# Kernel optimization log

Hardware: AMD Instinct MI355X
Metric: run time of the kernel (lower is better)

Reference implementation:

```python
import jax, jax.numpy as jnp
import numpy as np

D = 512; H = 8; DH = D // H; NB = 4; DMLP = 2048; L = 32; ROPE_DIM = 32
SCALE = DH ** -0.25  # scale_exponent = -0.25, applied to both q and k
EPS = 1e-6


def _rms(x, g):
    return x * jax.lax.rsqrt(jnp.mean(x * x, axis=-1, keepdims=True) + EPS) * g


def _rope_tables(T):
    inv = 1.0 / (10000.0 ** (jnp.arange(0, ROPE_DIM, 2, dtype=jnp.float32) / ROPE_DIM))
    ang = jnp.arange(T, dtype=jnp.float32)[:, None] * inv[None, :]  # (T, ROPE_DIM/2)
    return jnp.cos(ang), jnp.sin(ang)


def _apply_rope(x, cos, sin):
    # x: (N, H, T, DH); rotate first ROPE_DIM dims, interleaved pairs
    xr, rest = x[..., :ROPE_DIM], x[..., ROPE_DIM:]
    x1, x2 = xr[..., 0::2], xr[..., 1::2]
    c = cos[None, None]; s = sin[None, None]
    r1 = x1 * c - x2 * s
    r2 = x1 * s + x2 * c
    rot = jnp.stack([r1, r2], axis=-1).reshape(xr.shape)
    return jnp.concatenate([rot, rest], axis=-1)


def _mha(q_in, kv_in, wq, wk, bk, wv, wo, rope=None):
    # q_in: (N, Lq, D), kv_in: (N, Lk, D); k has bias, q/v/o do not
    N, Lq, _ = q_in.shape
    Lk = kv_in.shape[1]
    q = (q_in @ wq).reshape(N, Lq, H, DH).transpose(0, 2, 1, 3)
    k = (kv_in @ wk + bk).reshape(N, Lk, H, DH).transpose(0, 2, 1, 3)
    v = (kv_in @ wv).reshape(N, Lk, H, DH).transpose(0, 2, 1, 3)
    if rope is not None:
        cos, sin = rope
        q = _apply_rope(q, cos, sin)
        k = _apply_rope(k, cos, sin)
    scores = jnp.einsum('nhqd,nhkd->nhqk', q * SCALE, k * SCALE)
    a = jax.nn.softmax(scores, axis=-1)
    o = jnp.einsum('nhqk,nhkd->nhqd', a, v).transpose(0, 2, 1, 3).reshape(N, Lq, D)
    return o @ wo


def _geglu_mlp(x, w1, w2):
    h = x @ w1                       # (..., 2*DMLP)
    a, g = jnp.split(h, 2, axis=-1)
    return (a * jax.nn.gelu(g)) @ w2


def setup_inputs() -> dict:
    key = jax.random.key(0)
    ks = jax.random.split(key, 16)
    w = lambda k, shape: jax.random.normal(k, shape, dtype=jnp.float32) * 0.02
    B, T, C = 8, 128, 64
    return {
        'source': jax.random.normal(ks[0], (B * T, C, D), dtype=jnp.float32),
        'query_latents': jax.random.normal(ks[1], (L, D), dtype=jnp.float32),
        'ca_ln': jnp.ones((NB, 3, D), jnp.float32),
        'ca_wq': w(ks[2], (NB, D, D)), 'ca_wk': w(ks[3], (NB, D, D)),
        'ca_bk': jnp.zeros((NB, D), jnp.float32),
        'ca_wv': w(ks[4], (NB, D, D)), 'ca_wo': w(ks[5], (NB, D, D)),
        'ca_w1': w(ks[6], (NB, D, 2 * DMLP)), 'ca_w2': w(ks[7], (NB, DMLP, D)),
        'ta_ln': jnp.ones((NB, 2, D), jnp.float32),
        'ta_wq': w(ks[8], (NB, D, D)), 'ta_wk': w(ks[9], (NB, D, D)),
        'ta_bk': jnp.zeros((NB, D), jnp.float32),
        'ta_wv': w(ks[10], (NB, D, D)), 'ta_wo': w(ks[11], (NB, D, D)),
        'ta_w1': w(ks[12], (NB, D, 2 * DMLP)), 'ta_w2': w(ks[13], (NB, DMLP, D)),
        'B': B, 'T': T,
    }


def reference(source, query_latents, ca_ln, ca_wq, ca_wk, ca_bk, ca_wv, ca_wo,
              ca_w1, ca_w2, ta_ln, ta_wq, ta_wk, ta_bk, ta_wv, ta_wo, ta_w1,
              ta_w2, B, T):
    BT = source.shape[0]
    rope = _rope_tables(T)
    latents = jnp.broadcast_to(query_latents[None], (BT, L, D))
    for b in range(NB):
        # --- PerceiverResamplerBlock (spatial cross-attn) ---
        l_n = _rms(latents, ca_ln[b, 0])
        s_n = _rms(source, ca_ln[b, 1])
        kv = jnp.concatenate([s_n, l_n], axis=1)  # (BT, C+L, D)
        latents = latents + _mha(l_n, kv, ca_wq[b], ca_wk[b], ca_bk[b], ca_wv[b], ca_wo[b])
        latents = latents + _geglu_mlp(_rms(latents, ca_ln[b, 2]), ca_w1[b], ca_w2[b])
        # --- TemporalAttentionBlock: (B T) L D -> (B L) T D ---
        x = latents.reshape(B, T, L, D).transpose(0, 2, 1, 3).reshape(B * L, T, D)
        x_n = _rms(x, ta_ln[b, 0])
        x = x + _mha(x_n, x_n, ta_wq[b], ta_wk[b], ta_bk[b], ta_wv[b], ta_wo[b], rope=rope)
        x = x + _geglu_mlp(_rms(x, ta_ln[b, 1]), ta_w1[b], ta_w2[b])
        latents = x.reshape(B, L, T, D).transpose(0, 2, 1, 3).reshape(BT, L, D)
    # '(B T) L D -> B T (L D)'
    return latents.reshape(B, T, L * D)
```

## Files before the change

kernel.cpp:

```cpp
#include <hip/hip_runtime.h>
#include <stdint.h>


typedef short    bf16x8 __attribute__((ext_vector_type(8)));
typedef float    f32x4  __attribute__((ext_vector_type(4)));
typedef uint16_t u16;

__device__ __forceinline__ float bf2f(uint32_t u) {
  union { uint32_t i; float f; } x; x.i = u << 16; return x.f;
}
__device__ __forceinline__ u16 f2bf(float f) {
  union { float f; uint32_t i; } x; x.f = f;
  return (u16)((x.i + 0x7fffu + ((x.i >> 16) & 1u)) >> 16);
}
__device__ __forceinline__ float gelu_t(float x) {
  float u = 0.7978845608028654f * (x + 0.044715f * x * x * x);
  float t = 1.f - 2.f / (__expf(2.f * u) + 1.f);
  return 0.5f * x * (1.f + t);
}
template<int RMAP>
__device__ __forceinline__ int maprow(int r) {
  if (RMAP == 0) return r;
  int b = r >> 12, rem = r & 4095;
  return ((b << 7) + (rem & 127)) * 32 + (rem >> 7);
}
__device__ __forceinline__ void glds16(const u16* g, u16* l) {
  __builtin_amdgcn_global_load_lds((const __attribute__((address_space(1))) uint32_t*)(g),
                                   (__attribute__((address_space(3))) uint32_t*)(l),
                                   16, 0, 0);
}

__global__ __launch_bounds__(256) void transpose_cast(const float* __restrict__ src,
                                                      u16* __restrict__ dst,
                                                      int R, int C, size_t zsD) {
  src += (size_t)blockIdx.z * R * C;
  dst += (size_t)blockIdx.z * zsD;
  __shared__ float t[32][33];
  int c0 = blockIdx.x * 32, r0 = blockIdx.y * 32;
  int tx = threadIdx.x & 31, ty = threadIdx.x >> 5;
#pragma unroll
  for (int i = 0; i < 32; i += 8) t[ty + i][tx] = src[(size_t)(r0 + ty + i) * C + c0 + tx];
  __syncthreads();
#pragma unroll
  for (int i = 0; i < 32; i += 8)
    dst[(size_t)(c0 + ty + i) * R + r0 + tx] = f2bf(t[tx][ty + i]);
}

__global__ __launch_bounds__(256) void transpose_w1(const float* __restrict__ src,
                                                    u16* __restrict__ dst) {
  src += (size_t)blockIdx.z * 512 * 4096;
  dst += (size_t)blockIdx.z * 512 * 4096;
  __shared__ float t[32][33];
  int c0 = blockIdx.x * 32, r0 = blockIdx.y * 32;
  int m0 = (c0 >> 8) * 128 + ((c0 >> 6) & 3) * 32 + ((c0 & 32) ? 2048 : 0);
  int tx = threadIdx.x & 31, ty = threadIdx.x >> 5;
#pragma unroll
  for (int i = 0; i < 32; i += 8) t[ty + i][tx] = src[(size_t)(r0 + ty + i) * 4096 + m0 + tx];
  __syncthreads();
#pragma unroll
  for (int i = 0; i < 32; i += 8)
    dst[(size_t)(c0 + ty + i) * 512 + r0 + tx] = f2bf(t[tx][ty + i]);
}

__global__ void rope_init(float* cosT, float* sinT) {
  int idx = blockIdx.x * 256 + threadIdx.x;
  if (idx < 128 * 16) {
    int t = idx >> 4, j = idx & 15;
    float inv = __expf(-logf(10000.f) * (float)j / 16.f);
    float a = (float)t * inv;
    cosT[idx] = cosf(a);
    sinT[idx] = sinf(a);
  }
}

__global__ __launch_bounds__(256) void init_lat(const float* __restrict__ ql,
                                                float* __restrict__ lat) {
  size_t i = (size_t)blockIdx.x * 256 + threadIdx.x;
  int r = (int)(i >> 7), cw = (int)(i & 127);
  int l = r & 31;
  ((float4*)lat)[i] = ((const float4*)ql)[l * 128 + cw];
}

template<int RMAP>
__global__ __launch_bounds__(256) void rms_rows(const float* __restrict__ src,
                                                const float* __restrict__ g,
                                                u16* __restrict__ out) {
  const int wid = threadIdx.x >> 6, lane = threadIdx.x & 63;
  const int row = (blockIdx.x << 2) + wid;
  const int srow = maprow<RMAP>(row);
  const float4* p = (const float4*)(src + (size_t)srow * 512);
  float4 v0 = p[lane * 2], v1 = p[lane * 2 + 1];
  float ss = v0.x * v0.x + v0.y * v0.y + v0.z * v0.z + v0.w * v0.w +
             v1.x * v1.x + v1.y * v1.y + v1.z * v1.z + v1.w * v1.w;
#pragma unroll
  for (int m = 1; m < 64; m <<= 1) ss += __shfl_xor(ss, m);
  const float rs = rsqrtf(ss * (1.f / 512.f) + 1e-6f);
  const float4* gp = (const float4*)g;
  float4 g0 = gp[lane * 2], g1 = gp[lane * 2 + 1];
  u16 rb[8];
  rb[0] = f2bf(v0.x * rs * g0.x); rb[1] = f2bf(v0.y * rs * g0.y);
  rb[2] = f2bf(v0.z * rs * g0.z); rb[3] = f2bf(v0.w * rs * g0.w);
  rb[4] = f2bf(v1.x * rs * g1.x); rb[5] = f2bf(v1.y * rs * g1.y);
  rb[6] = f2bf(v1.z * rs * g1.z); rb[7] = f2bf(v1.w * rs * g1.w);
  *(int4*)(out + (size_t)row * 512 + lane * 8) = *(int4*)rb;
}

template<int EPI, int RMAP, int AMAP>
__global__ __launch_bounds__(512, 2) void gemm256(const u16* __restrict__ A,
                                                  const u16* __restrict__ A2,
                                                  const u16* __restrict__ Bt,
                                                  u16* __restrict__ outH,
                                                  float* __restrict__ latF,
                                                  const float* __restrict__ bias,
                                                  int M, int N, int K, int nb) {
  __shared__ __align__(16) u16 Ab[3][256 * 64];
  __shared__ __align__(16) u16 Bb[2][256 * 64];
  const int tid = threadIdx.x;
  const int nwg = gridDim.x * gridDim.y;
  int bid = blockIdx.y * gridDim.x + blockIdx.x;
  bid = (bid & 7) * (nwg >> 3) + (bid >> 3);
  const int m0 = (bid / gridDim.x) << 8;
  const int n0 = (bid % gridDim.x) << 8;
  const int wid = tid >> 6, lane = tid & 63;
  const int wm = wid >> 2, wn = wid & 3;
  const int lr = lane & 15, lg = lane >> 4;
  const int rx = (lr & 7) << 3;

  auto stageA = [&](int slot, int kt, int h) {
#pragma unroll
    for (int i = 0; i < 2; ++i) {
      const int e = ((h * 2 + i) * 512 + tid) * 8;
      const int r = e >> 6;
      const int cs = (e & 63) ^ ((r & 7) << 3);
      const u16* src;
      if constexpr (AMAP == 0) {
        src = A + (size_t)(m0 + r) * K + kt * 64 + cs;
      } else {
        const int R = m0 + r;
        const int n_ = R / 96;
        const int j = R - n_ * 96;
        src = (j < 64) ? A  + ((size_t)((nb + n_) * 64 + j)) * 512 + kt * 64 + cs
                       : A2 + ((size_t)((nb + n_) * 32 + (j - 64))) * 512 + kt * 64 + cs;
      }
      glds16(src, &Ab[slot][e]);
    }
  };
  auto stageB = [&](int slot, int kt, int h) {
#pragma unroll
    for (int i = 0; i < 2; ++i) {
      const int e = ((h * 2 + i) * 512 + tid) * 8;
      const int r = e >> 6;
      const int cs = (e & 63) ^ ((r & 7) << 3);
      glds16(Bt + (size_t)(n0 + r) * K + kt * 64 + cs, &Bb[slot][e]);
    }
  };

  bf16x8 bfr[2][4];
  bf16x8 afrA[2][2], afrB_[2][2];
  auto readAfr = [&](bf16x8 (&dst)[2][2], const u16* Abase, int p) {
#pragma unroll
    for (int d = 0; d < 2; ++d)
#pragma unroll
      for (int ks = 0; ks < 2; ++ks) {
        const int rw = wm * 128 + (p * 2 + d) * 16 + lr;
        dst[d][ks] = *(const bf16x8*)&Abase[rw * 64 + ((ks * 32 + lg * 8) ^ rx)];
      }
  };
  auto readBfr = [&](const u16* Bbase) {
#pragma unroll
    for (int ks = 0; ks < 2; ++ks)
#pragma unroll
      for (int in = 0; in < 4; ++in) {
        const int rw = wn * 64 + in * 16 + lr;
        bfr[ks][in] = *(const bf16x8*)&Bbase[rw * 64 + ((ks * 32 + lg * 8) ^ rx)];
      }
  };

  f32x4 acc[8][4];
#pragma unroll
  for (int i = 0; i < 8; ++i)
#pragma unroll
    for (int j = 0; j < 4; ++j) acc[i][j] = (f32x4){0.f, 0.f, 0.f, 0.f};

  stageA(0, 0, 0); stageA(0, 0, 1);
  stageB(0, 0, 0); stageB(0, 0, 1);
  stageA(1, 1, 0); stageA(1, 1, 1);
  asm volatile("s_waitcnt vmcnt(4)" ::: "memory");
  __builtin_amdgcn_s_barrier();
  asm volatile("" ::: "memory");
  readBfr(&Bb[0][0]);
  readAfr(afrA, &Ab[0][0], 0);

  const int nkt = K >> 6;
  int sl0 = 0;
  int sl2 = 2;
  for (int kt = 0; kt < nkt; ++kt) {
    const u16* Abase = &Ab[sl0][0];
#pragma unroll
    for (int p = 0; p < 4; ++p) {
      if (p <= 1 && kt + 1 < nkt) stageB((kt + 1) & 1, kt + 1, p);
      if (p >= 2 && kt + 2 < nkt) stageA(sl2, kt + 2, p - 2);
      if (p < 3) {
        if ((p & 1) == 0) readAfr(afrB_, Abase, p + 1);
        else              readAfr(afrA,  Abase, p + 1);
      }
      __builtin_amdgcn_s_setprio(1);
      if ((p & 1) == 0) {
#pragma unroll
        for (int d = 0; d < 2; ++d)
#pragma unroll
          for (int in = 0; in < 4; ++in)
#pragma unroll
            for (int ks = 0; ks < 2; ++ks)
              acc[p * 2 + d][in] = __builtin_amdgcn_mfma_f32_16x16x32_bf16(
                  afrA[d][ks], bfr[ks][in], acc[p * 2 + d][in], 0, 0, 0);
      } else {
#pragma unroll
        for (int d = 0; d < 2; ++d)
#pragma unroll
          for (int in = 0; in < 4; ++in)
#pragma unroll
            for (int ks = 0; ks < 2; ++ks)
              acc[p * 2 + d][in] = __builtin_amdgcn_mfma_f32_16x16x32_bf16(
                  afrB_[d][ks], bfr[ks][in], acc[p * 2 + d][in], 0, 0, 0);
      }
      __builtin_amdgcn_s_setprio(0);
      if (p < 3) {
        __builtin_amdgcn_s_barrier();
      } else if (kt + 1 < nkt) {
        if (kt + 2 < nkt) asm volatile("s_waitcnt vmcnt(4)" ::: "memory");
        else              asm volatile("s_waitcnt vmcnt(0)" ::: "memory");
        __builtin_amdgcn_s_barrier();
        asm volatile("" ::: "memory");
        const int sln = (sl0 == 2) ? 0 : sl0 + 1;
        readBfr(&Bb[(kt + 1) & 1][0]);
        readAfr(afrA, &Ab[sln][0], 0);
      }
    }
    sl0 = (sl0 == 2) ? 0 : sl0 + 1;
    sl2 = (sl2 == 2) ? 0 : sl2 + 1;
  }

  if constexpr (EPI == 3) {
    const int t128 = n0 >> 1;
#pragma unroll
    for (int im = 0; im < 8; ++im)
#pragma unroll
      for (int in = 0; in < 2; ++in)
#pragma unroll
        for (int j = 0; j < 4; ++j) {
          const int row = m0 + wm * 128 + im * 16 + lg * 4 + j;
          const int hcol = t128 + wn * 32 + in * 16 + lr;
          outH[(size_t)row * 2048 + hcol] = f2bf(acc[im][in][j] * gelu_t(acc[im][in + 2][j]));
        }
  } else if constexpr (EPI == 2) {
#pragma unroll
    for (int im = 0; im < 8; ++im)
#pragma unroll
      for (int in = 0; in < 4; ++in) {
        const int col = n0 + wn * 64 + in * 16 + lr;
#pragma unroll
        for (int j = 0; j < 4; ++j) {
          const int row = m0 + wm * 128 + im * 16 + lg * 4 + j;
          const size_t rr = (size_t)maprow<RMAP>(row) * 512 + col;
          latF[rr] += acc[im][in][j];
        }
      }
  } else {
    float bv4[4];
    if constexpr (EPI == 1) {
#pragma unroll
      for (int in = 0; in < 4; ++in)
        bv4[in] = (n0 < 512) ? bias[n0 + wn * 64 + in * 16 + lr] : 0.f;
    }
#pragma unroll
    for (int im = 0; im < 8; ++im)
#pragma unroll
      for (int in = 0; in < 4; ++in) {
        const int col = n0 + wn * 64 + in * 16 + lr;
#pragma unroll
        for (int j = 0; j < 4; ++j) {
          const int row = m0 + wm * 128 + im * 16 + lg * 4 + j;
          float v = acc[im][in][j];
          if constexpr (EPI == 1) v += bv4[in];
          outH[(size_t)row * N + col] = f2bf(v);
        }
      }
  }
}

__global__ __launch_bounds__(256) void attn_ca(const u16* q,
                                               const u16* __restrict__ kv,
                                               u16* o, int nb) {
  union __align__(16) SM {
    struct { u16 Qs[32][72]; u16 Ks[96][72]; } qk;
    u16 Pb[32][104];
  };
  __shared__ SM sm;
  __shared__ __align__(16) u16 Vt[64][104];
  __shared__ float pmax[2][32];
  __shared__ float psum[2][32];
  const int nl = blockIdx.x, n = nb + nl, h = blockIdx.y, tid = threadIdx.x;

  {
    int r = tid >> 3, c = (tid & 7) * 8;
    *(int4*)&sm.qk.Qs[r][c] = *(const int4*)&q[((size_t)n * 32 + r) * 512 + h * 64 + c];
  }
#pragma unroll
  for (int i = 0; i < 3; ++i) {
    int idx = i * 256 + tid;
    int r = idx >> 3, c = (idx & 7) * 8;
    *(int4*)&sm.qk.Ks[r][c] = *(const int4*)&kv[((size_t)nl * 96 + r) * 1024 + h * 64 + c];
  }
#pragma unroll
  for (int i = 0; i < 3; ++i) {
    int idx = i * 256 + tid;
    int dg = idx / 96, t = idx - dg * 96;
    int4 pv = *(const int4*)&kv[((size_t)nl * 96 + t) * 1024 + 512 + h * 64 + dg * 8];
    const u16* pu = (const u16*)&pv;
#pragma unroll
    for (int e = 0; e < 8; ++e) Vt[dg * 8 + e][t] = pu[e];
  }
  __syncthreads();

  const int wid = tid >> 6, lane = tid & 63, lr = lane & 15, lg = lane >> 4;
  const int m0 = (wid & 1) * 16, wnq = wid >> 1, nbc = wnq * 48;

  f32x4 sa[3];
#pragma unroll
  for (int f = 0; f < 3; ++f) sa[f] = (f32x4){0.f, 0.f, 0.f, 0.f};
#pragma unroll
  for (int ks = 0; ks < 2; ++ks) {
    bf16x8 a = *(const bf16x8*)&sm.qk.Qs[m0 + lr][ks * 32 + lg * 8];
#pragma unroll
    for (int f = 0; f < 3; ++f) {
      bf16x8 bb = *(const bf16x8*)&sm.qk.Ks[nbc + f * 16 + lr][ks * 32 + lg * 8];
      sa[f] = __builtin_amdgcn_mfma_f32_16x16x32_bf16(a, bb, sa[f], 0, 0, 0);
    }
  }

#pragma unroll
  for (int j = 0; j < 4; ++j) {
    float m = fmaxf(fmaxf(sa[0][j], sa[1][j]), sa[2][j]);
    m = fmaxf(m, __shfl_xor(m, 1));
    m = fmaxf(m, __shfl_xor(m, 2));
    m = fmaxf(m, __shfl_xor(m, 4));
    m = fmaxf(m, __shfl_xor(m, 8));
    if (lr == 0) pmax[wnq][m0 + lg * 4 + j] = m;
  }
  __syncthreads();
#pragma unroll
  for (int j = 0; j < 4; ++j) {
    const int row = m0 + lg * 4 + j;
    const float m = fmaxf(pmax[0][row], pmax[1][row]);
    float s = 0.f;
#pragma unroll
    for (int f = 0; f < 3; ++f) {
      float p = __expf(0.125f * (sa[f][j] - m));
      sa[f][j] = p;
      s += p;
    }
    s += __shfl_xor(s, 1); s += __shfl_xor(s, 2); s += __shfl_xor(s, 4); s += __shfl_xor(s, 8);
    if (lr == 0) psum[wnq][row] = s;
  }
#pragma unroll
  for (int f = 0; f < 3; ++f)
#pragma unroll
    for (int j = 0; j < 4; ++j)
      sm.Pb[m0 + lg * 4 + j][nbc + f * 16 + lr] = f2bf(sa[f][j]);
  __syncthreads();

// ... 121 lines not shown
#pragma unroll
    for (int in = 0; in < 4; ++in)
#pragma unroll
      for (int j = 0; j < 4; ++j)
        sm.Pb[rbase + im * 16 + lg * 4 + j][wn * 64 + in * 16 + lr] = f2bf(sa[im][in][j]);
  __syncthreads();

  f32x4 oa[2][4];
#pragma unroll
  for (int i = 0; i < 2; ++i)
#pragma unroll
    for (int j = 0; j < 4; ++j) oa[i][j] = (f32x4){0.f, 0.f, 0.f, 0.f};
#pragma unroll
  for (int ks = 0; ks < 4; ++ks) {
    bf16x8 av[2], bv[4];
#pragma unroll
    for (int im = 0; im < 2; ++im)
      av[im] = *(const bf16x8*)&sm.Pb[wid * 32 + im * 16 + lr][ks * 32 + lg * 8];
#pragma unroll
    for (int in = 0; in < 4; ++in)
      bv[in] = *(const bf16x8*)&Vt[in * 16 + lr][ks * 32 + lg * 8];
#pragma unroll
    for (int im = 0; im < 2; ++im)
#pragma unroll
      for (int in = 0; in < 4; ++in)
        oa[im][in] = __builtin_amdgcn_mfma_f32_16x16x32_bf16(av[im], bv[in], oa[im][in], 0, 0, 0);
  }
#pragma unroll
  for (int im = 0; im < 2; ++im)
#pragma unroll
    for (int j = 0; j < 4; ++j) {
      const int qi = wid * 32 + im * 16 + lg * 4 + j;
      const float inv = 1.f / (psum[0][qi] + psum[1][qi]);
#pragma unroll
      for (int in = 0; in < 4; ++in)
        o[((size_t)n * 128 + qi) * 512 + h * 64 + in * 16 + lr] = f2bf(oa[im][in][j] * inv);
    }
}

extern "C" void kernel_launch(void* const* d_in, const int* in_sizes, int n_in,
                              void* d_out, int out_size, void* d_ws, size_t ws_size,
                              hipStream_t stream) {
  const float* source = (const float*)d_in[0];
  const float* qlat   = (const float*)d_in[1];
  const float* ca_ln  = (const float*)d_in[2];
  const float* ca_wq  = (const float*)d_in[3];
  const float* ca_wk  = (const float*)d_in[4];
  const float* ca_bk  = (const float*)d_in[5];
  const float* ca_wv  = (const float*)d_in[6];
  const float* ca_wo  = (const float*)d_in[7];
  const float* ca_w1  = (const float*)d_in[8];
  const float* ca_w2  = (const float*)d_in[9];
  const float* ta_ln  = (const float*)d_in[10];
  const float* ta_wq  = (const float*)d_in[11];
  const float* ta_wk  = (const float*)d_in[12];
  const float* ta_bk  = (const float*)d_in[13];
  const float* ta_wv  = (const float*)d_in[14];
  const float* ta_wo  = (const float*)d_in[15];
  const float* ta_w1  = (const float*)d_in[16];
  const float* ta_w2  = (const float*)d_in[17];
  float* lat = (float*)d_out;
  char* ws = (char*)d_ws;
  (void)in_sizes; (void)n_in; (void)out_size;

  if (ws_size < 251674624ull) return;

  const size_t WQ = 512 * 512, W1SZ = (size_t)512 * 4096, W2SZ = (size_t)2048 * 512;
  const size_t O_CA_WQ = 0,
               O_CA_KV = 4 * WQ,
               O_CA_WO = 12 * WQ,
               O_CA_W1 = 16 * WQ,
               O_CA_W2 = O_CA_W1 + 4 * W1SZ,
               O_TA_WQ = O_CA_W2 + 4 * W2SZ,
               O_TA_KV = O_TA_WQ + 4 * WQ,
               O_TA_WO = O_TA_KV + 8 * WQ,
               O_TA_W1 = O_TA_WO + 4 * WQ,
               O_TA_W2 = O_TA_W1 + 4 * W1SZ;

  u16*   W    = (u16*)ws;
  u16*   xn   = (u16*)(ws + 67108864);
  u16*   shat = (u16*)(ws + 100663296);
  u16*   qb   = (u16*)(ws + 167772160);
  u16*   kvb  = (u16*)(ws + 201326592);
  u16*   h2   = shat;
  u16*   takv = shat;
  float* cosT = (float*)(ws + 251658240);
  float* sinT = (float*)(ws + 251666432);

  transpose_cast<<<dim3(16, 16, 4), 256, 0, stream>>>(ca_wq, W + O_CA_WQ, 512, 512, WQ);
  transpose_cast<<<dim3(16, 16, 4), 256, 0, stream>>>(ca_wk, W + O_CA_KV, 512, 512, 2 * WQ);
  transpose_cast<<<dim3(16, 16, 4), 256, 0, stream>>>(ca_wv, W + O_CA_KV + WQ, 512, 512, 2 * WQ);
  transpose_cast<<<dim3(16, 16, 4), 256, 0, stream>>>(ca_wo, W + O_CA_WO, 512, 512, WQ);
  transpose_w1 <<<dim3(128, 16, 4), 256, 0, stream>>>(ca_w1, W + O_CA_W1);
  transpose_cast<<<dim3(16, 64, 4), 256, 0, stream>>>(ca_w2, W + O_CA_W2, 2048, 512, W2SZ);
  transpose_cast<<<dim3(16, 16, 4), 256, 0, stream>>>(ta_wq, W + O_TA_WQ, 512, 512, WQ);
  transpose_cast<<<dim3(16, 16, 4), 256, 0, stream>>>(ta_wk, W + O_TA_KV, 512, 512, 2 * WQ);
  transpose_cast<<<dim3(16, 16, 4), 256, 0, stream>>>(ta_wv, W + O_TA_KV + WQ, 512, 512, 2 * WQ);
  transpose_cast<<<dim3(16, 16, 4), 256, 0, stream>>>(ta_wo, W + O_TA_WO, 512, 512, WQ);
  transpose_w1 <<<dim3(128, 16, 4), 256, 0, stream>>>(ta_w1, W + O_TA_W1);
  transpose_cast<<<dim3(16, 64, 4), 256, 0, stream>>>(ta_w2, W + O_TA_W2, 2048, 512, W2SZ);
  rope_init<<<8, 256, 0, stream>>>(cosT, sinT);
  init_lat<<<16384, 256, 0, stream>>>(qlat, lat);

  for (int b = 0; b < 4; ++b) {
    const u16* wqt   = W + O_CA_WQ + (size_t)b * WQ;
    const u16* wkvt  = W + O_CA_KV + (size_t)b * 2 * WQ;
    const u16* wot   = W + O_CA_WO + (size_t)b * WQ;
    const u16* w1t   = W + O_CA_W1 + (size_t)b * W1SZ;
    const u16* w2t   = W + O_CA_W2 + (size_t)b * W2SZ;
    const u16* twqt  = W + O_TA_WQ + (size_t)b * WQ;
    const u16* twkvt = W + O_TA_KV + (size_t)b * 2 * WQ;
    const u16* twot  = W + O_TA_WO + (size_t)b * WQ;
    const u16* tw1t  = W + O_TA_W1 + (size_t)b * W1SZ;
    const u16* tw2t  = W + O_TA_W2 + (size_t)b * W2SZ;

    rms_rows<0><<<8192, 256, 0, stream>>>(lat, ca_ln + b * 1536, xn);
    rms_rows<0><<<16384, 256, 0, stream>>>(source, ca_ln + b * 1536 + 512, shat);
    gemm256<0, 0, 0><<<dim3(2, 128), 512, 0, stream>>>(xn, nullptr, wqt, qb, nullptr, nullptr, 32768, 512, 512, 0);
    for (int c = 0; c < 4; ++c) {
      gemm256<1, 0, 1><<<dim3(4, 96), 512, 0, stream>>>(shat, xn, wkvt, kvb, nullptr, ca_bk + b * 512, 24576, 1024, 512, c * 256);
      attn_ca<<<dim3(256, 8), 256, 0, stream>>>(qb, kvb, qb, c * 256);
    }
    gemm256<2, 0, 0><<<dim3(2, 128), 512, 0, stream>>>(qb, nullptr, wot, nullptr, lat, nullptr, 32768, 512, 512, 0);
    rms_rows<0><<<8192, 256, 0, stream>>>(lat, ca_ln + b * 1536 + 1024, xn);
    gemm256<3, 0, 0><<<dim3(16, 128), 512, 0, stream>>>(xn, nullptr, w1t, h2, nullptr, nullptr, 32768, 4096, 512, 0);
    gemm256<2, 0, 0><<<dim3(2, 128), 512, 0, stream>>>(h2, nullptr, w2t, nullptr, lat, nullptr, 32768, 512, 2048, 0);

    rms_rows<1><<<8192, 256, 0, stream>>>(lat, ta_ln + b * 1024, xn);
    gemm256<0, 0, 0><<<dim3(2, 128), 512, 0, stream>>>(xn, nullptr, twqt, qb, nullptr, nullptr, 32768, 512, 512, 0);
    gemm256<1, 0, 0><<<dim3(4, 128), 512, 0, stream>>>(xn, nullptr, twkvt, takv, nullptr, ta_bk + b * 512, 32768, 1024, 512, 0);
    attn_ta<<<dim3(256, 8), 256, 0, stream>>>(qb, takv, cosT, sinT, qb);
    gemm256<2, 1, 0><<<dim3(2, 128), 512, 0, stream>>>(qb, nullptr, twot, nullptr, lat, nullptr, 32768, 512, 512, 0);
    rms_rows<1><<<8192, 256, 0, stream>>>(lat, ta_ln + b * 1024 + 512, xn);
    gemm256<3, 0, 0><<<dim3(16, 128), 512, 0, stream>>>(xn, nullptr, tw1t, h2, nullptr, nullptr, 32768, 4096, 512, 0);
    gemm256<2, 1, 0><<<dim3(2, 128), 512, 0, stream>>>(h2, nullptr, tw2t, nullptr, lat, nullptr, 32768, 512, 2048, 0);
  }
}
```

Measured before the change: 4.910 ms.

## Fuse GeGLU MLP up-projection, gating and down-projection into one kernel

Replaces the two-GEMM MLP (W1 with GeGLU epilogue writing a bf16 hidden buffer, then W2 accumulating into latents) with a single kernel. Each block owns 128 rows, loops over 16 hidden chunks of 128, keeps the gated chunk in LDS and accumulates the W2 product in registers. This removes the 32768x2048 hidden tensor round-trip through global memory and one launch. In exchange the new kernel uses a simpler double-buffered pipeline with full vmcnt(0) barriers, launches only 256 blocks, and rereads the full W1/W2 weights per block.

```diff
diff --git a/kernel.cpp b/kernel.cpp
--- a/kernel.cpp
+++ b/kernel.cpp
@@ -28,6 +28,11 @@
   __builtin_amdgcn_global_load_lds((const __attribute__((address_space(1))) uint32_t*)(g),
                                    (__attribute__((address_space(3))) uint32_t*)(l),
                                    16, 0, 0);
+}
+__device__ __forceinline__ void vm0_bar() {
+  asm volatile("s_waitcnt vmcnt(0)" ::: "memory");
+  __builtin_amdgcn_s_barrier();
+  asm volatile("" ::: "memory");
 }
 
 __global__ __launch_bounds__(256) void transpose_cast(const float* __restrict__ src,
@@ -52,7 +57,7 @@
   dst += (size_t)blockIdx.z * 512 * 4096;
   __shared__ float t[32][33];
   int c0 = blockIdx.x * 32, r0 = blockIdx.y * 32;
-  int m0 = (c0 >> 8) * 128 + ((c0 >> 6) & 3) * 32 + ((c0 & 32) ? 2048 : 0);
+  int m0 = (c0 >> 8) * 128 + (((c0 >> 6) & 3)) * 32 + ((c0 >> 5) & 1) * 2048;
   int tx = threadIdx.x & 31, ty = threadIdx.x >> 5;
 #pragma unroll
   for (int i = 0; i < 32; i += 8) t[ty + i][tx] = src[(size_t)(r0 + ty + i) * 4096 + m0 + tx];
@@ -103,6 +108,141 @@
   rb[4] = f2bf(v1.x * rs * g1.x); rb[5] = f2bf(v1.y * rs * g1.y);
   rb[6] = f2bf(v1.z * rs * g1.z); rb[7] = f2bf(v1.w * rs * g1.w);
   *(int4*)(out + (size_t)row * 512 + lane * 8) = *(int4*)rb;
+}
+
+template<int RMAP>
+__global__ __launch_bounds__(512, 2) void mlp_fused(const u16* __restrict__ A,
+                                                    const u16* __restrict__ W1t,
+                                                    const u16* __restrict__ W2t,
+                                                    float* __restrict__ latF) {
+  __shared__ union __align__(16) {
+    struct { u16 Ab[2][128 * 64]; u16 B1b[2][256 * 64]; } g1;
+    struct { u16 B2b[2][512 * 32]; } g2;
+  } stg;
+  __shared__ __align__(16) u16 hb[128][136];
+  const int tid = threadIdx.x;
+  const int bid = blockIdx.x;
+  const int rb = (((bid & 7) << 5) + (bid >> 3)) << 7;
+  const int wid = tid >> 6, lane = tid & 63;
+  const int wm = wid >> 2, wn = wid & 3;
+  const int lr = lane & 15, lg = lane >> 4;
+  const int rx = (lr & 7) << 3;
+
+  auto stageA1 = [&](int bf, int kt) {
+#pragma unroll
+    for (int i = 0; i < 2; ++i) {
+      const int e = (i * 512 + tid) * 8;
+      const int r = e >> 6;
+      const int cs = (e & 63) ^ ((r & 7) << 3);
+      glds16(A + (size_t)(rb + r) * 512 + kt * 64 + cs, &stg.g1.Ab[bf][e]);
+    }
+  };
+  f32x4 acc2[4][8];
+#pragma unroll
+  for (int i = 0; i < 4; ++i)
+#pragma unroll
+    for (int j = 0; j < 8; ++j) acc2[i][j] = (f32x4){0.f, 0.f, 0.f, 0.f};
+
+  for (int c = 0; c < 16; ++c) {
+    auto stageB1 = [&](int bf, int kt) {
+#pragma unroll
+      for (int i = 0; i < 4; ++i) {
+        const int e = (i * 512 + tid) * 8;
+        const int r = e >> 6;
+        const int cs = (e & 63) ^ ((r & 7) << 3);
+        glds16(W1t + (size_t)(c * 256 + r) * 512 + kt * 64 + cs, &stg.g1.B1b[bf][e]);
+      }
+    };
+    auto stageB2 = [&](int bf, int kt2) {
+#pragma unroll
+      for (int i = 0; i < 4; ++i) {
+        const int e = (i * 512 + tid) * 8;
+        const int r = e >> 5;
+        const int cs = (e & 31) ^ (((r >> 1) & 3) << 3);
+        glds16(W2t + (size_t)r * 2048 + c * 128 + kt2 * 32 + cs, &stg.g2.B2b[bf][e]);
+      }
+    };
+
+    f32x4 acc1[4][4];
+#pragma unroll
+    for (int i = 0; i < 4; ++i)
+#pragma unroll
+      for (int j = 0; j < 4; ++j) acc1[i][j] = (f32x4){0.f, 0.f, 0.f, 0.f};
+    stageA1(0, 0); stageB1(0, 0);
+    vm0_bar();
+    for (int kt = 0; kt < 8; ++kt) {
+      const int bf = kt & 1;
+      if (kt + 1 < 8) { stageA1(bf ^ 1, kt + 1); stageB1(bf ^ 1, kt + 1); }
+      const u16* Ab_ = &stg.g1.Ab[bf][0];
+      const u16* Bb_ = &stg.g1.B1b[bf][0];
+#pragma unroll
+      for (int ks = 0; ks < 2; ++ks) {
+        bf16x8 av[4], bv[4];
+#pragma unroll
+        for (int im = 0; im < 4; ++im)
+          av[im] = *(const bf16x8*)&Ab_[(wm * 64 + im * 16 + lr) * 64 + ((ks * 32 + lg * 8) ^ rx)];
+#pragma unroll
+        for (int in = 0; in < 4; ++in)
+          bv[in] = *(const bf16x8*)&Bb_[(wn * 64 + in * 16 + lr) * 64 + ((ks * 32 + lg * 8) ^ rx)];
+        __builtin_amdgcn_s_setprio(1);
+#pragma unroll
+        for (int im = 0; im < 4; ++im)
+#pragma unroll
+          for (int in = 0; in < 4; ++in)
+            acc1[im][in] = __builtin_amdgcn_mfma_f32_16x16x32_bf16(av[im], bv[in], acc1[im][in], 0, 0, 0);
+        __builtin_amdgcn_s_setprio(0);
+      }
+      vm0_bar();
+    }
+
+#pragma unroll
+    for (int im = 0; im < 4; ++im)
+#pragma unroll
+      for (int in = 0; in < 2; ++in)
+#pragma unroll
+        for (int j = 0; j < 4; ++j) {
+          const int row = wm * 64 + im * 16 + lg * 4 + j;
+          const int hl = wn * 32 + in * 16 + lr;
+          hb[row][hl] = f2bf(acc1[im][in][j] * gelu_t(acc1[im][in + 2][j]));
+        }
+    stageB2(0, 0);
+    __syncthreads();
+
+    for (int kt2 = 0; kt2 < 4; ++kt2) {
+      const int bf = kt2 & 1;
+      if (kt2 + 1 < 4) stageB2(bf ^ 1, kt2 + 1);
+      const u16* B2_ = &stg.g2.B2b[bf][0];
+      bf16x8 av[4], bv[8];
+#pragma unroll
+      for (int im = 0; im < 4; ++im)
+        av[im] = *(const bf16x8*)&hb[wm * 64 + im * 16 + lr][kt2 * 32 + lg * 8];
+#pragma unroll
+      for (int in = 0; in < 8; ++in) {
+        const int ng = wn * 128 + in * 16 + lr;
+        bv[in] = *(const bf16x8*)&B2_[ng * 32 + ((lg * 8) ^ (((ng >> 1) & 3) << 3))];
+      }
+      __builtin_amdgcn_s_setprio(1);
+#pragma unroll
+      for (int im = 0; im < 4; ++im)
+#pragma unroll
+        for (int in = 0; in < 8; ++in)
+          acc2[im][in] = __builtin_amdgcn_mfma_f32_16x16x32_bf16(av[im], bv[in], acc2[im][in], 0, 0, 0);
+      __builtin_amdgcn_s_setprio(0);
+      vm0_bar();
+    }
+  }
+
+#pragma unroll
+  for (int im = 0; im < 4; ++im)
+#pragma unroll
+    for (int in = 0; in < 8; ++in) {
+      const int col = wn * 128 + in * 16 + lr;
+#pragma unroll
+      for (int j = 0; j < 4; ++j) {
+        const int row = rb + wm * 64 + im * 16 + lg * 4 + j;
+        latF[(size_t)maprow<RMAP>(row) * 512 + col] += acc2[im][in][j];
+      }
+    }
 }
 
 template<int EPI, int RMAP, int AMAP>
@@ -192,8 +332,7 @@
   readAfr(afrA, &Ab[0][0], 0);
 
   const int nkt = K >> 6;
-  int sl0 = 0;
-  int sl2 = 2;
+  int sl0 = 0, sl2 = 2;
   for (int kt = 0; kt < nkt; ++kt) {
     const u16* Abase = &Ab[sl0][0];
 #pragma unroll
@@ -241,19 +380,7 @@
     sl2 = (sl2 == 2) ? 0 : sl2 + 1;
   }
 
-  if constexpr (EPI == 3) {
-    const int t128 = n0 >> 1;
-#pragma unroll
-    for (int im = 0; im < 8; ++im)
-#pragma unroll
-      for (int in = 0; in < 2; ++in)
-#pragma unroll
-        for (int j = 0; j < 4; ++j) {
-          const int row = m0 + wm * 128 + im * 16 + lg * 4 + j;
-          const int hcol = t128 + wn * 32 + in * 16 + lr;
-          outH[(size_t)row * 2048 + hcol] = f2bf(acc[im][in][j] * gelu_t(acc[im][in + 2][j]));
-        }
-  } else if constexpr (EPI == 2) {
+  if constexpr (EPI == 2) {
 #pragma unroll
     for (int im = 0; im < 8; ++im)
 #pragma unroll
@@ -574,7 +701,6 @@
   u16*   shat = (u16*)(ws + 100663296);
   u16*   qb   = (u16*)(ws + 167772160);
   u16*   kvb  = (u16*)(ws + 201326592);
-  u16*   h2   = shat;
   u16*   takv = shat;
   float* cosT = (float*)(ws + 251658240);
   float* sinT = (float*)(ws + 251666432);
@@ -615,8 +741,7 @@
     }
     gemm256<2, 0, 0><<<dim3(2, 128), 512, 0, stream>>>(qb, nullptr, wot, nullptr, lat, nullptr, 32768, 512, 512, 0);
     rms_rows<0><<<8192, 256, 0, stream>>>(lat, ca_ln + b * 1536 + 1024, xn);
-    gemm256<3, 0, 0><<<dim3(16, 128), 512, 0, stream>>>(xn, nullptr, w1t, h2, nullptr, nullptr, 32768, 4096, 512, 0);
-    gemm256<2, 0, 0><<<dim3(2, 128), 512, 0, stream>>>(h2, nullptr, w2t, nullptr, lat, nullptr, 32768, 512, 2048, 0);
+    mlp_fused<0><<<256, 512, 0, stream>>>(xn, w1t, w2t, lat);
 
     rms_rows<1><<<8192, 256, 0, stream>>>(lat, ta_ln + b * 1024, xn);
     gemm256<0, 0, 0><<<dim3(2, 128), 512, 0, stream>>>(xn, nullptr, twqt, qb, nullptr, nullptr, 32768, 512, 512, 0);
@@ -624,7 +749,6 @@
     attn_ta<<<dim3(256, 8), 256, 0, stream>>>(qb, takv, cosT, sinT, qb);
     gemm256<2, 1, 0><<<dim3(2, 128), 512, 0, stream>>>(qb, nullptr, twot, nullptr, lat, nullptr, 32768, 512, 512, 0);
     rms_rows<1><<<8192, 256, 0, stream>>>(lat, ta_ln + b * 1024 + 512, xn);
-    gemm256<3, 0, 0><<<dim3(16, 128), 512, 0, stream>>>(xn, nullptr, tw1t, h2, nullptr, nullptr, 32768, 4096, 512, 0);
-    gemm256<2, 1, 0><<<dim3(2, 128), 512, 0, stream>>>(h2, nullptr, tw2t, nullptr, lat, nullptr, 32768, 512, 2048, 0);
-  }
-}
+    mlp_fused<1><<<256, 512, 0, stream>>>(xn, tw1t, tw2t, lat);
+  }
+}
```

New measurement: 6.023 ms. 1.23x slower.

## Make GEMM kernel persistent over multiple tiles with cross-tile prefetch pipeline

Applied to the files above, without the earlier changes.

Turns the 256x256 GEMM into a semi-persistent kernel where each workgroup processes TPB consecutive output tiles as one flattened virtual K loop. The next tile's A/B loads are prefetched while the current tile finishes, and the epilogue runs mid-loop before the accumulators are reset. This removes per-tile prologue and pipeline drain, and shrinks the grid to 256 or 192 workgroups, intended to match the CU count. The cost is that the epilogue stores now sit inside the pipelined loop and can stall MFMA issue. Tile order within a workgroup also changes L2 reuse.

```diff
diff --git a/kernel.cpp b/kernel.cpp
--- a/kernel.cpp
+++ b/kernel.cpp
@@ -105,28 +105,33 @@
   *(int4*)(out + (size_t)row * 512 + lane * 8) = *(int4*)rb;
 }
 
-template<int EPI, int RMAP, int AMAP>
-__global__ __launch_bounds__(512, 2) void gemm256(const u16* __restrict__ A,
-                                                  const u16* __restrict__ A2,
-                                                  const u16* __restrict__ Bt,
-                                                  u16* __restrict__ outH,
-                                                  float* __restrict__ latF,
-                                                  const float* __restrict__ bias,
-                                                  int M, int N, int K, int nb) {
+template<int EPI, int RMAP, int AMAP, int TPB>
+__global__ __launch_bounds__(512, 2) void gemm256p(const u16* __restrict__ A,
+                                                   const u16* __restrict__ A2,
+                                                   const u16* __restrict__ Bt,
+                                                   u16* __restrict__ outH,
+                                                   float* __restrict__ latF,
+                                                   const float* __restrict__ bias,
+                                                   int N, int K, int ltn, int nb) {
   __shared__ __align__(16) u16 Ab[3][256 * 64];
   __shared__ __align__(16) u16 Bb[2][256 * 64];
   const int tid = threadIdx.x;
-  const int nwg = gridDim.x * gridDim.y;
-  int bid = blockIdx.y * gridDim.x + blockIdx.x;
-  bid = (bid & 7) * (nwg >> 3) + (bid >> 3);
-  const int m0 = (bid / gridDim.x) << 8;
-  const int n0 = (bid % gridDim.x) << 8;
+  const int NBk = gridDim.x;
+  const int sb = (blockIdx.x & 7) * (NBk >> 3) + (blockIdx.x >> 3);
   const int wid = tid >> 6, lane = tid & 63;
   const int wm = wid >> 2, wn = wid & 3;
   const int lr = lane & 15, lg = lane >> 4;
   const int rx = (lr & 7) << 3;
-
-  auto stageA = [&](int slot, int kt, int h) {
+  const int nkt = K >> 6;
+  const int lnkt = __builtin_ctz(nkt);
+  const int tmask = nkt - 1;
+  const int NV = TPB * nkt;
+  const int tnm = (1 << ltn) - 1;
+
+  auto stageA = [&](int vk, int slot, int h) {
+    const int g = sb * TPB + (vk >> lnkt);
+    const int m0 = (g >> ltn) << 8;
+    const int kt = vk & tmask;
 #pragma unroll
     for (int i = 0; i < 2; ++i) {
       const int e = ((h * 2 + i) * 512 + tid) * 8;
@@ -145,7 +150,10 @@
       glds16(src, &Ab[slot][e]);
     }
   };
-  auto stageB = [&](int slot, int kt, int h) {
+  auto stageB = [&](int vk, int slot, int h) {
+    const int g = sb * TPB + (vk >> lnkt);
+    const int n0 = (g & tnm) << 8;
+    const int kt = vk & tmask;
 #pragma unroll
     for (int i = 0; i < 2; ++i) {
       const int e = ((h * 2 + i) * 512 + tid) * 8;
@@ -181,6 +189,58 @@
   for (int i = 0; i < 8; ++i)
 #pragma unroll
     for (int j = 0; j < 4; ++j) acc[i][j] = (f32x4){0.f, 0.f, 0.f, 0.f};
+
+  auto epilogue = [&](int tv) {
+    const int g = sb * TPB + tv;
+    const int m0 = (g >> ltn) << 8;
+    const int n0 = (g & tnm) << 8;
+    if constexpr (EPI == 3) {
+      const int t128 = n0 >> 1;
+#pragma unroll
+      for (int im = 0; im < 8; ++im)
+#pragma unroll
+        for (int in = 0; in < 2; ++in)
+#pragma unroll
+          for (int j = 0; j < 4; ++j) {
+            const int row = m0 + wm * 128 + im * 16 + lg * 4 + j;
+            const int hcol = t128 + wn * 32 + in * 16 + lr;
+            outH[(size_t)row * 2048 + hcol] = f2bf(acc[im][in][j] * gelu_t(acc[im][in + 2][j]));
+          }
+    } else if constexpr (EPI == 2) {
+#pragma unroll
+      for (int im = 0; im < 8; ++im)
+#pragma unroll
+        for (int in = 0; in < 4; ++in) {
+          const int col = n0 + wn * 64 + in * 16 + lr;
+#pragma unroll
+          for (int j = 0; j < 4; ++j) {
+            const int row = m0 + wm * 128 + im * 16 + lg * 4 + j;
+            const size_t rr = (size_t)maprow<RMAP>(row) * 512 + col;
+            latF[rr] += acc[im][in][j];
+          }
+        }
+    } else {
+      float bv4[4];
+      if constexpr (EPI == 1) {
+#pragma unroll
+        for (int in = 0; in < 4; ++in)
+          bv4[in] = (n0 < 512) ? bias[n0 + wn * 64 + in * 16 + lr] : 0.f;
+      }
+#pragma unroll
+      for (int im = 0; im < 8; ++im)
+#pragma unroll
+        for (int in = 0; in < 4; ++in) {
+          const int col = n0 + wn * 64 + in * 16 + lr;
+#pragma unroll
+          for (int j = 0; j < 4; ++j) {
+            const int row = m0 + wm * 128 + im * 16 + lg * 4 + j;
+            float v = acc[im][in][j];
+            if constexpr (EPI == 1) v += bv4[in];
+            outH[(size_t)row * N + col] = f2bf(v);
+          }
+        }
+    }
+  };
 
   stageA(0, 0, 0); stageA(0, 0, 1);
   stageB(0, 0, 0); stageB(0, 0, 1);
@@ -191,15 +251,13 @@
   readBfr(&Bb[0][0]);
   readAfr(afrA, &Ab[0][0], 0);
 
-  const int nkt = K >> 6;
-  int sl0 = 0;
-  int sl2 = 2;
-  for (int kt = 0; kt < nkt; ++kt) {
+  int sl0 = 0, sl2 = 2;
+  for (int vk = 0; vk < NV; ++vk) {
     const u16* Abase = &Ab[sl0][0];
 #pragma unroll
     for (int p = 0; p < 4; ++p) {
-      if (p <= 1 && kt + 1 < nkt) stageB((kt + 1) & 1, kt + 1, p);
-      if (p >= 2 && kt + 2 < nkt) stageA(sl2, kt + 2, p - 2);
+      if (p <= 1 && vk + 1 < NV) stageB(vk + 1, (vk + 1) & 1, p);
+      if (p >= 2 && vk + 2 < NV) stageA(vk + 2, sl2, p - 2);
       if (p < 3) {
         if ((p & 1) == 0) readAfr(afrB_, Abase, p + 1);
         else              readAfr(afrA,  Abase, p + 1);
@@ -227,66 +285,27 @@
       __builtin_amdgcn_s_setprio(0);
       if (p < 3) {
         __builtin_amdgcn_s_barrier();
-      } else if (kt + 1 < nkt) {
-        if (kt + 2 < nkt) asm volatile("s_waitcnt vmcnt(4)" ::: "memory");
-        else              asm volatile("s_waitcnt vmcnt(0)" ::: "memory");
+      } else if (vk + 1 < NV) {
+        if (vk + 2 < NV) asm volatile("s_waitcnt vmcnt(4)" ::: "memory");
+        else             asm volatile("s_waitcnt vmcnt(0)" ::: "memory");
         __builtin_amdgcn_s_barrier();
         asm volatile("" ::: "memory");
+        if (TPB > 1 && (vk & tmask) == tmask) {
+          epilogue(vk >> lnkt);
+#pragma unroll
+          for (int i = 0; i < 8; ++i)
+#pragma unroll
+            for (int j = 0; j < 4; ++j) acc[i][j] = (f32x4){0.f, 0.f, 0.f, 0.f};
+        }
         const int sln = (sl0 == 2) ? 0 : sl0 + 1;
-        readBfr(&Bb[(kt + 1) & 1][0]);
+        readBfr(&Bb[(vk + 1) & 1][0]);
         readAfr(afrA, &Ab[sln][0], 0);
       }
     }
     sl0 = (sl0 == 2) ? 0 : sl0 + 1;
     sl2 = (sl2 == 2) ? 0 : sl2 + 1;
   }
-
-  if constexpr (EPI == 3) {
-    const int t128 = n0 >> 1;
-#pragma unroll
-    for (int im = 0; im < 8; ++im)
-#pragma unroll
-      for (int in = 0; in < 2; ++in)
-#pragma unroll
-        for (int j = 0; j < 4; ++j) {
-          const int row = m0 + wm * 128 + im * 16 + lg * 4 + j;
-          const int hcol = t128 + wn * 32 + in * 16 + lr;
-          outH[(size_t)row * 2048 + hcol] = f2bf(acc[im][in][j] * gelu_t(acc[im][in + 2][j]));
-        }
-  } else if constexpr (EPI == 2) {
-#pragma unroll
-    for (int im = 0; im < 8; ++im)
-#pragma unroll
-      for (int in = 0; in < 4; ++in) {
-        const int col = n0 + wn * 64 + in * 16 + lr;
-#pragma unroll
-        for (int j = 0; j < 4; ++j) {
-          const int row = m0 + wm * 128 + im * 16 + lg * 4 + j;
-          const size_t rr = (size_t)maprow<RMAP>(row) * 512 + col;
-          latF[rr] += acc[im][in][j];
-        }
-      }
-  } else {
-    float bv4[4];
-    if constexpr (EPI == 1) {
-#pragma unroll
-      for (int in = 0; in < 4; ++in)
-        bv4[in] = (n0 < 512) ? bias[n0 + wn * 64 + in * 16 + lr] : 0.f;
-    }
-#pragma unroll
-    for (int im = 0; im < 8; ++im)
-#pragma unroll
-      for (int in = 0; in < 4; ++in) {
-        const int col = n0 + wn * 64 + in * 16 + lr;
-#pragma unroll
-        for (int j = 0; j < 4; ++j) {
-          const int row = m0 + wm * 128 + im * 16 + lg * 4 + j;
-          float v = acc[im][in][j];
-          if constexpr (EPI == 1) v += bv4[in];
-          outH[(size_t)row * N + col] = f2bf(v);
-        }
-      }
-  }
+  epilogue(TPB - 1);
 }
 
 __global__ __launch_bounds__(256) void attn_ca(const u16* q,
@@ -608,23 +627,23 @@
 
     rms_rows<0><<<8192, 256, 0, stream>>>(lat, ca_ln + b * 1536, xn);
     rms_rows<0><<<16384, 256, 0, stream>>>(source, ca_ln + b * 1536 + 512, shat);
-    gemm256<0, 0, 0><<<dim3(2, 128), 512, 0, stream>>>(xn, nullptr, wqt, qb, nullptr, nullptr, 32768, 512, 512, 0);
+    gemm256p<0, 0, 0, 1><<<256, 512, 0, stream>>>(xn, nullptr, wqt, qb, nullptr, nullptr, 512, 512, 1, 0);
     for (int c = 0; c < 4; ++c) {
-      gemm256<1, 0, 1><<<dim3(4, 96), 512, 0, stream>>>(shat, xn, wkvt, kvb, nullptr, ca_bk + b * 512, 24576, 1024, 512, c * 256);
+      gemm256p<1, 0, 1, 2><<<192, 512, 0, stream>>>(shat, xn, wkvt, kvb, nullptr, ca_bk + b * 512, 1024, 512, 2, c * 256);
       attn_ca<<<dim3(256, 8), 256, 0, stream>>>(qb, kvb, qb, c * 256);
     }
-    gemm256<2, 0, 0><<<dim3(2, 128), 512, 0, stream>>>(qb, nullptr, wot, nullptr, lat, nullptr, 32768, 512, 512, 0);
+    gemm256p<2, 0, 0, 1><<<256, 512, 0, stream>>>(qb, nullptr, wot, nullptr, lat, nullptr, 512, 512, 1, 0);
     rms_rows<0><<<8192, 256, 0, stream>>>(lat, ca_ln + b * 1536 + 1024, xn);
-    gemm256<3, 0, 0><<<dim3(16, 128), 512, 0, stream>>>(xn, nullptr, w1t, h2, nullptr, nullptr, 32768, 4096, 512, 0);
-    gemm256<2, 0, 0><<<dim3(2, 128), 512, 0, stream>>>(h2, nullptr, w2t, nullptr, lat, nullptr, 32768, 512, 2048, 0);
+    gemm256p<3, 0, 0, 8><<<256, 512, 0, stream>>>(xn, nullptr, w1t, h2, nullptr, nullptr, 4096, 512, 4, 0);
+    gemm256p<2, 0, 0, 1><<<256, 512, 0, stream>>>(h2, nullptr, w2t, nullptr, lat, nullptr, 512, 2048, 1, 0);
 
     rms_rows<1><<<8192, 256, 0, stream>>>(lat, ta_ln + b * 1024, xn);
-    gemm256<0, 0, 0><<<dim3(2, 128), 512, 0, stream>>>(xn, nullptr, twqt, qb, nullptr, nullptr, 32768, 512, 512, 0);
-    gemm256<1, 0, 0><<<dim3(4, 128), 512, 0, stream>>>(xn, nullptr, twkvt, takv, nullptr, ta_bk + b * 512, 32768, 1024, 512, 0);
+    gemm256p<0, 0, 0, 1><<<256, 512, 0, stream>>>(xn, nullptr, twqt, qb, nullptr, nullptr, 512, 512, 1, 0);
+    gemm256p<1, 0, 0, 2><<<256, 512, 0, stream>>>(xn, nullptr, twkvt, takv, nullptr, ta_bk + b * 512, 1024, 512, 2, 0);
     attn_ta<<<dim3(256, 8), 256, 0, stream>>>(qb, takv, cosT, sinT, qb);
-    gemm256<2, 1, 0><<<dim3(2, 128), 512, 0, stream>>>(qb, nullptr, twot, nullptr, lat, nullptr, 32768, 512, 512, 0);
+    gemm256p<2, 1, 0, 1><<<256, 512, 0, stream>>>(qb, nullptr, twot, nullptr, lat, nullptr, 512, 512, 1, 0);
     rms_rows<1><<<8192, 256, 0, stream>>>(lat, ta_ln + b * 1024 + 512, xn);
-    gemm256<3, 0, 0><<<dim3(16, 128), 512, 0, stream>>>(xn, nullptr, tw1t, h2, nullptr, nullptr, 32768, 4096, 512, 0);
-    gemm256<2, 1, 0><<<dim3(2, 128), 512, 0, stream>>>(h2, nullptr, tw2t, nullptr, lat, nullptr, 32768, 512, 2048, 0);
-  }
-}
+    gemm256p<3, 0, 0, 8><<<256, 512, 0, stream>>>(xn, nullptr, tw1t, h2, nullptr, nullptr, 4096, 512, 4, 0);
+    gemm256p<2, 1, 0, 1><<<256, 512, 0, stream>>>(h2, nullptr, tw2t, nullptr, lat, nullptr, 512, 2048, 1, 0);
+  }
+}
```

After: 5.207 ms. 1.06x slower.

## Switch GEMM to double-buffered A with fewer barriers and a 1D grid

Applied to the files above, without the earlier changes.

Rewrites the GEMM main loop to double-buffer A (two LDS slots instead of three) and prefetch only one k-tile ahead, unrolled by two for static slot indices. It also removes the per-phase barriers and uses a 1D grid with shift-based tile decode instead of divides. The aim is less LDS use and fewer barriers, at the cost of a shallower prefetch that may expose global load latency. Each k-step now waits with vmcnt(0) before its barrier.

```diff
diff --git a/kernel.cpp b/kernel.cpp
--- a/kernel.cpp
+++ b/kernel.cpp
@@ -106,27 +106,27 @@
 }
 
 template<int EPI, int RMAP, int AMAP>
-__global__ __launch_bounds__(512, 2) void gemm256(const u16* __restrict__ A,
-                                                  const u16* __restrict__ A2,
-                                                  const u16* __restrict__ Bt,
-                                                  u16* __restrict__ outH,
-                                                  float* __restrict__ latF,
-                                                  const float* __restrict__ bias,
-                                                  int M, int N, int K, int nb) {
-  __shared__ __align__(16) u16 Ab[3][256 * 64];
+__global__ __launch_bounds__(512, 2) void gemm256d(const u16* __restrict__ A,
+                                                   const u16* __restrict__ A2,
+                                                   const u16* __restrict__ Bt,
+                                                   u16* __restrict__ outH,
+                                                   float* __restrict__ latF,
+                                                   const float* __restrict__ bias,
+                                                   int N, int K, int ltn, int nb) {
+  __shared__ __align__(16) u16 Ab[2][256 * 64];
   __shared__ __align__(16) u16 Bb[2][256 * 64];
   const int tid = threadIdx.x;
-  const int nwg = gridDim.x * gridDim.y;
-  int bid = blockIdx.y * gridDim.x + blockIdx.x;
-  bid = (bid & 7) * (nwg >> 3) + (bid >> 3);
-  const int m0 = (bid / gridDim.x) << 8;
-  const int n0 = (bid % gridDim.x) << 8;
+  const int NBk = gridDim.x;
+  const int sb = (blockIdx.x & 7) * (NBk >> 3) + (blockIdx.x >> 3);
+  const int m0 = (sb >> ltn) << 8;
+  const int n0 = (sb & ((1 << ltn) - 1)) << 8;
   const int wid = tid >> 6, lane = tid & 63;
   const int wm = wid >> 2, wn = wid & 3;
   const int lr = lane & 15, lg = lane >> 4;
   const int rx = (lr & 7) << 3;
-
-  auto stageA = [&](int slot, int kt, int h) {
+  const int nkt = K >> 6;
+
+  auto stageA = [&](int kt, int slot, int h) {
 #pragma unroll
     for (int i = 0; i < 2; ++i) {
       const int e = ((h * 2 + i) * 512 + tid) * 8;
@@ -145,7 +145,7 @@
       glds16(src, &Ab[slot][e]);
     }
   };
-  auto stageB = [&](int slot, int kt, int h) {
+  auto stageB = [&](int kt, int slot, int h) {
 #pragma unroll
     for (int i = 0; i < 2; ++i) {
       const int e = ((h * 2 + i) * 512 + tid) * 8;
@@ -184,61 +184,56 @@
 
   stageA(0, 0, 0); stageA(0, 0, 1);
   stageB(0, 0, 0); stageB(0, 0, 1);
-  stageA(1, 1, 0); stageA(1, 1, 1);
-  asm volatile("s_waitcnt vmcnt(4)" ::: "memory");
+  asm volatile("s_waitcnt vmcnt(0)" ::: "memory");
   __builtin_amdgcn_s_barrier();
   asm volatile("" ::: "memory");
   readBfr(&Bb[0][0]);
   readAfr(afrA, &Ab[0][0], 0);
 
-  const int nkt = K >> 6;
-  int sl0 = 0;
-  int sl2 = 2;
-  for (int kt = 0; kt < nkt; ++kt) {
-    const u16* Abase = &Ab[sl0][0];
-#pragma unroll
-    for (int p = 0; p < 4; ++p) {
-      if (p <= 1 && kt + 1 < nkt) stageB((kt + 1) & 1, kt + 1, p);
-      if (p >= 2 && kt + 2 < nkt) stageA(sl2, kt + 2, p - 2);
-      if (p < 3) {
-        if ((p & 1) == 0) readAfr(afrB_, Abase, p + 1);
-        else              readAfr(afrA,  Abase, p + 1);
+  for (int kt0 = 0; kt0 < nkt; kt0 += 2) {
+#pragma unroll
+    for (int par = 0; par < 2; ++par) {
+      const int vk = kt0 + par;
+      const u16* Abase = &Ab[par][0];
+      const bool pf = (vk + 1 < nkt);
+#pragma unroll
+      for (int p = 0; p < 4; ++p) {
+        if (p == 0 && pf) { stageB(vk + 1, par ^ 1, 0); stageB(vk + 1, par ^ 1, 1); }
+        if (p == 1 && pf) { stageA(vk + 1, par ^ 1, 0); stageA(vk + 1, par ^ 1, 1); }
+        if (p < 3) {
+          if ((p & 1) == 0) readAfr(afrB_, Abase, p + 1);
+          else              readAfr(afrA,  Abase, p + 1);
+        }
+        __builtin_amdgcn_s_setprio(1);
+        if ((p & 1) == 0) {
+#pragma unroll
+          for (int d = 0; d < 2; ++d)
+#pragma unroll
+            for (int in = 0; in < 4; ++in)
+#pragma unroll
+              for (int ks = 0; ks < 2; ++ks)
+                acc[p * 2 + d][in] = __builtin_amdgcn_mfma_f32_16x16x32_bf16(
+                    afrA[d][ks], bfr[ks][in], acc[p * 2 + d][in], 0, 0, 0);
+        } else {
+#pragma unroll
+          for (int d = 0; d < 2; ++d)
+#pragma unroll
+            for (int in = 0; in < 4; ++in)
+#pragma unroll
+              for (int ks = 0; ks < 2; ++ks)
+                acc[p * 2 + d][in] = __builtin_amdgcn_mfma_f32_16x16x32_bf16(
+                    afrB_[d][ks], bfr[ks][in], acc[p * 2 + d][in], 0, 0, 0);
+        }
+        __builtin_amdgcn_s_setprio(0);
+        if (p == 3 && pf) {
+          asm volatile("s_waitcnt vmcnt(0)" ::: "memory");
+          __builtin_amdgcn_s_barrier();
+          asm volatile("" ::: "memory");
+          readBfr(&Bb[par ^ 1][0]);
+          readAfr(afrA, &Ab[par ^ 1][0], 0);
+        }
       }
-      __builtin_amdgcn_s_setprio(1);
-      if ((p & 1) == 0) {
-#pragma unroll
-        for (int d = 0; d < 2; ++d)
-#pragma unroll
-          for (int in = 0; in < 4; ++in)
-#pragma unroll
-            for (int ks = 0; ks < 2; ++ks)
-              acc[p * 2 + d][in] = __builtin_amdgcn_mfma_f32_16x16x32_bf16(
-                  afrA[d][ks], bfr[ks][in], acc[p * 2 + d][in], 0, 0, 0);
-      } else {
-#pragma unroll
-        for (int d = 0; d < 2; ++d)
-#pragma unroll
-          for (int in = 0; in < 4; ++in)
-#pragma unroll
-            for (int ks = 0; ks < 2; ++ks)
-              acc[p * 2 + d][in] = __builtin_amdgcn_mfma_f32_16x16x32_bf16(
-                  afrB_[d][ks], bfr[ks][in], acc[p * 2 + d][in], 0, 0, 0);
-      }
-      __builtin_amdgcn_s_setprio(0);
-      if (p < 3) {
-        __builtin_amdgcn_s_barrier();
-      } else if (kt + 1 < nkt) {
-        if (kt + 2 < nkt) asm volatile("s_waitcnt vmcnt(4)" ::: "memory");
-        else              asm volatile("s_waitcnt vmcnt(0)" ::: "memory");
-        __builtin_amdgcn_s_barrier();
-        asm volatile("" ::: "memory");
-        const int sln = (sl0 == 2) ? 0 : sl0 + 1;
-        readBfr(&Bb[(kt + 1) & 1][0]);
-        readAfr(afrA, &Ab[sln][0], 0);
-      }
-    }
-    sl0 = (sl0 == 2) ? 0 : sl0 + 1;
-    sl2 = (sl2 == 2) ? 0 : sl2 + 1;
+    }
   }
 
   if constexpr (EPI == 3) {
@@ -608,23 +603,23 @@
 
     rms_rows<0><<<8192, 256, 0, stream>>>(lat, ca_ln + b * 1536, xn);
     rms_rows<0><<<16384, 256, 0, stream>>>(source, ca_ln + b * 1536 + 512, shat);
-    gemm256<0, 0, 0><<<dim3(2, 128), 512, 0, stream>>>(xn, nullptr, wqt, qb, nullptr, nullptr, 32768, 512, 512, 0);
+    gemm256d<0, 0, 0><<<256, 512, 0, stream>>>(xn, nullptr, wqt, qb, nullptr, nullptr, 512, 512, 1, 0);
     for (int c = 0; c < 4; ++c) {
-      gemm256<1, 0, 1><<<dim3(4, 96), 512, 0, stream>>>(shat, xn, wkvt, kvb, nullptr, ca_bk + b * 512, 24576, 1024, 512, c * 256);
+      gemm256d<1, 0, 1><<<384, 512, 0, stream>>>(shat, xn, wkvt, kvb, nullptr, ca_bk + b * 512, 1024, 512, 2, c * 256);
       attn_ca<<<dim3(256, 8), 256, 0, stream>>>(qb, kvb, qb, c * 256);
     }
-    gemm256<2, 0, 0><<<dim3(2, 128), 512, 0, stream>>>(qb, nullptr, wot, nullptr, lat, nullptr, 32768, 512, 512, 0);
+    gemm256d<2, 0, 0><<<256, 512, 0, stream>>>(qb, nullptr, wot, nullptr, lat, nullptr, 512, 512, 1, 0);
     rms_rows<0><<<8192, 256, 0, stream>>>(lat, ca_ln + b * 1536 + 1024, xn);
-    gemm256<3, 0, 0><<<dim3(16, 128), 512, 0, stream>>>(xn, nullptr, w1t, h2, nullptr, nullptr, 32768, 4096, 512, 0);
-    gemm256<2, 0, 0><<<dim3(2, 128), 512, 0, stream>>>(h2, nullptr, w2t, nullptr, lat, nullptr, 32768, 512, 2048, 0);
+    gemm256d<3, 0, 0><<<2048, 512, 0, stream>>>(xn, nullptr, w1t, h2, nullptr, nullptr, 4096, 512, 4, 0);
+    gemm256d<2, 0, 0><<<256, 512, 0, stream>>>(h2, nullptr, w2t, nullptr, lat, nullptr, 512, 2048, 1, 0);
 
     rms_rows<1><<<8192, 256, 0, stream>>>(lat, ta_ln + b * 1024, xn);
-    gemm256<0, 0, 0><<<dim3(2, 128), 512, 0, stream>>>(xn, nullptr, twqt, qb, nullptr, nullptr, 32768, 512, 512, 0);
-    gemm256<1, 0, 0><<<dim3(4, 128), 512, 0, stream>>>(xn, nullptr, twkvt, takv, nullptr, ta_bk + b * 512, 32768, 1024, 512, 0);
+    gemm256d<0, 0, 0><<<256, 512, 0, stream>>>(xn, nullptr, twqt, qb, nullptr, nullptr, 512, 512, 1, 0);
+    gemm256d<1, 0, 0><<<512, 512, 0, stream>>>(xn, nullptr, twkvt, takv, nullptr, ta_bk + b * 512, 1024, 512, 2, 0);
     attn_ta<<<dim3(256, 8), 256, 0, stream>>>(qb, takv, cosT, sinT, qb);
-    gemm256<2, 1, 0><<<dim3(2, 128), 512, 0, stream>>>(qb, nullptr, twot, nullptr, lat, nullptr, 32768, 512, 512, 0);
+    gemm256d<2, 1, 0><<<256, 512, 0, stream>>>(qb, nullptr, twot, nullptr, lat, nullptr, 512, 512, 1, 0);
     rms_rows<1><<<8192, 256, 0, stream>>>(lat, ta_ln + b * 1024 + 512, xn);
-    gemm256<3, 0, 0><<<dim3(16, 128), 512, 0, stream>>>(xn, nullptr, tw1t, h2, nullptr, nullptr, 32768, 4096, 512, 0);
-    gemm256<2, 1, 0><<<dim3(2, 128), 512, 0, stream>>>(h2, nullptr, tw2t, nullptr, lat, nullptr, 32768, 512, 2048, 0);
-  }
-}
+    gemm256d<3, 0, 0><<<2048, 512, 0, stream>>>(xn, nullptr, tw1t, h2, nullptr, nullptr, 4096, 512, 4, 0);
+    gemm256d<2, 1, 0><<<256, 512, 0, stream>>>(h2, nullptr, tw2t, nullptr, lat, nullptr, 512, 2048, 1, 0);
+  }
+}
```

Measured after the change: 4.436 ms. -9.6%, faster.
